# Kernel tuning notes

Measured on AMD Instinct MI355X. Metric: run time of the kernel, lower is better.

The kernel has to match this reference:

```python
import jax, jax.numpy as jnp
import numpy as np
from jax import lax

B, T, D_MODEL = 4, 2048, 2048
EXPAND, D_CONV = 2, 4
D_INNER = D_MODEL * EXPAND


def setup_inputs() -> dict:
    key = jax.random.key(0)
    ks = jax.random.split(key, 5)
    x = jax.random.normal(ks[0], (B, T, D_MODEL), dtype=jnp.float32)
    w_in = jax.random.normal(ks[1], (2 * D_INNER, D_MODEL), dtype=jnp.float32) * (D_MODEL ** -0.5)
    w_out = jax.random.normal(ks[2], (D_MODEL, D_INNER), dtype=jnp.float32) * (D_INNER ** -0.5)
    conv_w = jax.random.normal(ks[3], (D_INNER, 1, D_CONV), dtype=jnp.float32) * (D_CONV ** -0.5)
    conv_b = jax.random.normal(ks[4], (D_INNER,), dtype=jnp.float32) * 0.02
    D = jnp.ones((D_INNER,), dtype=jnp.float32)
    return {"x": x, "w_in": w_in, "w_out": w_out, "conv_w": conv_w, "conv_b": conv_b, "D": D}


def _forward(x, w_in, w_out, conv_w, conv_b, D):
    # in_proj: [B,T,C] @ [C, 2*d_inner]
    x_proj = jnp.einsum('btc,dc->btd', x, w_in)
    xi, gate = jnp.split(x_proj, 2, axis=-1)  # each [B,T,d_inner]
    # depthwise causal conv1d: torch pads both sides by d_conv-1 then truncates
    # output to first T positions -> equivalent to left-pad (d_conv-1), valid conv.
    xc = jnp.transpose(xi, (0, 2, 1))  # [B, d_inner, T]
    xc = lax.conv_general_dilated(
        xc, conv_w,
        window_strides=(1,),
        padding=[(D_CONV - 1, 0)],
        dimension_numbers=('NCH', 'OIH', 'NCH'),
        feature_group_count=D_INNER,
    ) + conv_b[None, :, None]
    xc = jnp.transpose(xc, (0, 2, 1))  # [B, T, d_inner]
    h = jax.nn.silu(xc) * D[None, None, :] * jax.nn.silu(gate)
    return jnp.einsum('btd,cd->btc', h, w_out)


def reference(x, w_in, w_out, conv_w, conv_b, D):
    return _forward(x, w_in, w_out, conv_w, conv_b, D)
```

## Files before the change

### kernel.cpp

```cpp
#include <hip/hip_runtime.h>
#include <hip/hip_bf16.h>
#include <stdint.h>


#define BT_TOTAL 8192
#define DM 2048
#define DI 4096

typedef __attribute__((ext_vector_type(8))) short short8;
typedef __attribute__((ext_vector_type(4))) float f32x4;

__device__ __forceinline__ void async_ld16(const void* g, void* l) {
    __builtin_amdgcn_global_load_lds(
        (__attribute__((address_space(1))) void*)g,
        (__attribute__((address_space(3))) void*)l,
        16, 0, 0);
}

template<bool OUT_BF16>
__global__ __launch_bounds__(256) void gemm_bt_kernel(
    const ushort* __restrict__ A, const ushort* __restrict__ B,
    void* __restrict__ Cp, int M, int N, int K)
{
    __shared__ ushort As[128 * 64];
    __shared__ ushort Bs[128 * 64];

    const int tid  = threadIdx.x;
    const int lane = tid & 63;
    const int wave = tid >> 6;
    const int wm   = (wave >> 1) * 64;
    const int wn   = (wave & 1) * 64;
    const int lr   = lane & 15;
    const int quad = lane >> 4;

    const int bm = blockIdx.y * 128;
    const int bn = blockIdx.x * 128;

    f32x4 acc[4][4];
#pragma unroll
    for (int i = 0; i < 4; ++i)
#pragma unroll
        for (int j = 0; j < 4; ++j)
            acc[i][j] = (f32x4){0.f, 0.f, 0.f, 0.f};

    const ushort* ag[4];
    const ushort* bg[4];
    ushort* al[4];
    ushort* bl[4];
#pragma unroll
    for (int t = 0; t < 4; ++t) {
        const int c  = tid + t * 256;
        const int r  = c >> 3;
        const int co = ((c & 7) ^ (r & 7)) * 8;
        ag[t] = A + (size_t)(bm + r) * (size_t)K + co;
        bg[t] = B + (size_t)(bn + r) * (size_t)K + co;
        al[t] = &As[c * 8];
        bl[t] = &Bs[c * 8];
    }

    for (int kk = 0; kk < K; kk += 64) {
        __syncthreads();
#pragma unroll
        for (int t = 0; t < 4; ++t) {
            async_ld16(ag[t] + kk, al[t]);
            async_ld16(bg[t] + kk, bl[t]);
        }
        __syncthreads();

#pragma unroll
        for (int ks = 0; ks < 64; ks += 32) {
            const int ca = ((quad + (ks >> 3)) ^ (lr & 7)) * 8;
            short8 af[4], bfr[4];
#pragma unroll
            for (int mt = 0; mt < 4; ++mt)
                af[mt] = *(const short8*)&As[(wm + mt * 16 + lr) * 64 + ca];
#pragma unroll
            for (int nt = 0; nt < 4; ++nt)
                bfr[nt] = *(const short8*)&Bs[(wn + nt * 16 + lr) * 64 + ca];
#pragma unroll
            for (int mt = 0; mt < 4; ++mt)
#pragma unroll
                for (int nt = 0; nt < 4; ++nt)
                    acc[mt][nt] = __builtin_amdgcn_mfma_f32_16x16x32_bf16(
                        af[mt], bfr[nt], acc[mt][nt], 0, 0, 0);
        }
    }

    const int row0 = bm + wm + quad * 4;
    const int col0 = bn + wn + lr;
    if (OUT_BF16) {
        __hip_bfloat16* C = (__hip_bfloat16*)Cp;
#pragma unroll
        for (int mt = 0; mt < 4; ++mt)
#pragma unroll
            for (int r = 0; r < 4; ++r) {
                const int gr = row0 + mt * 16 + r;
                __hip_bfloat16* Crow = C + (size_t)gr * (size_t)N + col0;
#pragma unroll
                for (int nt = 0; nt < 4; ++nt)
                    Crow[nt * 16] = __float2bfloat16(acc[mt][nt][r]);
            }
    } else {
        float* C = (float*)Cp;
#pragma unroll
        for (int mt = 0; mt < 4; ++mt)
#pragma unroll
            for (int r = 0; r < 4; ++r) {
                const int gr = row0 + mt * 16 + r;
                float* Crow = C + (size_t)gr * (size_t)N + col0;
#pragma unroll
                for (int nt = 0; nt < 4; ++nt)
                    Crow[nt * 16] = acc[mt][nt][r];
            }
    }
}

__global__ __launch_bounds__(256) void conv_silu_kernel(
    const __hip_bfloat16* __restrict__ xp,
    const float* __restrict__ cw,
    const float* __restrict__ cb,
    const float* __restrict__ Dv,
    __hip_bfloat16* __restrict__ h)
{
    const int idx = blockIdx.x * 256 + threadIdx.x;
    const int d  = idx & (DI - 1);
    const int bt = idx >> 12;
    const int t  = bt & 2047;

    const float gate = __bfloat162float(xp[(size_t)bt * (2 * DI) + DI + d]);

    float a = cb[d];
    const float4 w = *(const float4*)(cw + d * 4);
    const float wk[4] = {w.x, w.y, w.z, w.w};
#pragma unroll
    for (int k = 0; k < 4; ++k) {
        const int tt = t - 3 + k;
        if (tt >= 0)
            a += __bfloat162float(xp[(size_t)(bt - 3 + k) * (2 * DI) + d]) * wk[k];
    }
    const float sc = a / (1.f + __expf(-a));
    const float sg = gate / (1.f + __expf(-gate));
    h[(size_t)bt * DI + d] = __float2bfloat16(sc * Dv[d] * sg);
}

__global__ __launch_bounds__(256) void f32_to_bf16_x4(
    const float* __restrict__ in, __hip_bfloat16* __restrict__ out, int n4)
{
    const int i = blockIdx.x * 256 + threadIdx.x;
    if (i >= n4) return;
    const float4 v = *(const float4*)(in + (size_t)i * 4);
    union { __hip_bfloat16 hh[4]; ushort4 u; } cv;
    cv.hh[0] = __float2bfloat16(v.x);
    cv.hh[1] = __float2bfloat16(v.y);
    cv.hh[2] = __float2bfloat16(v.z);
    cv.hh[3] = __float2bfloat16(v.w);
    *(ushort4*)((ushort*)out + (size_t)i * 4) = cv.u;
}

extern "C" void kernel_launch(void* const* d_in, const int* in_sizes, int n_in,
                              void* d_out, int out_size, void* d_ws, size_t ws_size,
                              hipStream_t stream)
{
    const float* x     = (const float*)d_in[0];
    const float* w_in  = (const float*)d_in[1];
    const float* w_out = (const float*)d_in[2];
    const float* cw    = (const float*)d_in[3];
    const float* cb    = (const float*)d_in[4];
    const float* Dv    = (const float*)d_in[5];
    float* out = (float*)d_out;

    char* wsc = (char*)d_ws;
    __hip_bfloat16* xproj = (__hip_bfloat16*)wsc;
    __hip_bfloat16* xb    = (__hip_bfloat16*)(wsc + (size_t)134217728);
    __hip_bfloat16* winb  = (__hip_bfloat16*)(wsc + (size_t)134217728 + 33554432);
    __hip_bfloat16* hbuf  = (__hip_bfloat16*)(wsc + (size_t)134217728);
    __hip_bfloat16* woutb = (__hip_bfloat16*)(wsc + (size_t)201326592);

    f32_to_bf16_x4<<<(BT_TOTAL * DM / 4 + 255) / 256, 256, 0, stream>>>(x, xb, BT_TOTAL * DM / 4);
    f32_to_bf16_x4<<<(2 * DI * DM / 4 + 255) / 256, 256, 0, stream>>>(w_in, winb, 2 * DI * DM / 4);
    f32_to_bf16_x4<<<(DM * DI / 4 + 255) / 256, 256, 0, stream>>>(w_out, woutb, DM * DI / 4);

    gemm_bt_kernel<true><<<dim3(2 * DI / 128, BT_TOTAL / 128), 256, 0, stream>>>(
        (const ushort*)xb, (const ushort*)winb, xproj, BT_TOTAL, 2 * DI, DM);

    conv_silu_kernel<<<(BT_TOTAL * DI) / 256, 256, 0, stream>>>(xproj, cw, cb, Dv, hbuf);

    gemm_bt_kernel<false><<<dim3(DM / 128, BT_TOTAL / 128), 256, 0, stream>>>(
        (const ushort*)hbuf, (const ushort*)woutb, out, BT_TOTAL, DM, DI);
}
```

Baseline: 740.7 us.

## Use 32x32x16 MFMA in GEMMs and vectorize conv-SiLU kernel by eight

```diff
diff --git a/kernel.cpp b/kernel.cpp
--- a/kernel.cpp
+++ b/kernel.cpp
@@ -1,14 +1,15 @@
 #include <hip/hip_runtime.h>
 #include <hip/hip_bf16.h>
 #include <stdint.h>
+#include <string.h>
 
 
 #define BT_TOTAL 8192
 #define DM 2048
 #define DI 4096
 
-typedef __attribute__((ext_vector_type(8))) short short8;
-typedef __attribute__((ext_vector_type(4))) float f32x4;
+typedef __attribute__((ext_vector_type(8)))  short short8;
+typedef __attribute__((ext_vector_type(16))) float f32x16;
 
 __device__ __forceinline__ void async_ld16(const void* g, void* l) {
     __builtin_amdgcn_global_load_lds(
@@ -17,6 +18,16 @@
         16, 0, 0);
 }
 
+__device__ __forceinline__ float bf2f(ushort u) {
+    union { uint i; float f; } v; v.i = ((uint)u) << 16; return v.f;
+}
+
+__device__ __forceinline__ ushort f2bf_bits(float f) {
+    union { __hip_bfloat16 b; ushort u; } v;
+    v.b = __float2bfloat16(f);
+    return v.u;
+}
+
 template<bool OUT_BF16>
 __global__ __launch_bounds__(256) void gemm_bt_kernel(
     const ushort* __restrict__ A, const ushort* __restrict__ B,
@@ -30,21 +41,22 @@
     const int wave = tid >> 6;
     const int wm   = (wave >> 1) * 64;
     const int wn   = (wave & 1) * 64;
-    const int lr   = lane & 15;
-    const int quad = lane >> 4;
+    const int l31  = lane & 31;
+    const int half = lane >> 5;
 
     const int bm = blockIdx.y * 128;
     const int bn = blockIdx.x * 128;
 
-    f32x4 acc[4][4];
-#pragma unroll
-    for (int i = 0; i < 4; ++i)
-#pragma unroll
-        for (int j = 0; j < 4; ++j)
-            acc[i][j] = (f32x4){0.f, 0.f, 0.f, 0.f};
-
-    const ushort* ag[4];
-    const ushort* bg[4];
+    f32x16 acc[2][2];
+#pragma unroll
+    for (int i = 0; i < 2; ++i)
+#pragma unroll
+        for (int j = 0; j < 2; ++j)
+#pragma unroll
+            for (int r = 0; r < 16; ++r)
+                acc[i][j][r] = 0.f;
+
+    int aoff[4], boff[4];
     ushort* al[4];
     ushort* bl[4];
 #pragma unroll
@@ -52,95 +64,132 @@
         const int c  = tid + t * 256;
         const int r  = c >> 3;
         const int co = ((c & 7) ^ (r & 7)) * 8;
-        ag[t] = A + (size_t)(bm + r) * (size_t)K + co;
-        bg[t] = B + (size_t)(bn + r) * (size_t)K + co;
+        aoff[t] = (bm + r) * K + co;
+        boff[t] = (bn + r) * K + co;
         al[t] = &As[c * 8];
         bl[t] = &Bs[c * 8];
     }
 
+    const ushort* aP[8];
+    const ushort* bP[8];
+#pragma unroll
+    for (int s = 0; s < 4; ++s)
+#pragma unroll
+        for (int tt = 0; tt < 2; ++tt) {
+            const int rowA = wm + tt * 32 + l31;
+            const int rowB = wn + tt * 32 + l31;
+            const int q = s * 2 + half;
+            aP[s * 2 + tt] = &As[rowA * 64 + (q ^ (rowA & 7)) * 8];
+            bP[s * 2 + tt] = &Bs[rowB * 64 + (q ^ (rowB & 7)) * 8];
+        }
+
     for (int kk = 0; kk < K; kk += 64) {
+        const ushort* Ak = A + kk;
+        const ushort* Bk = B + kk;
         __syncthreads();
 #pragma unroll
         for (int t = 0; t < 4; ++t) {
-            async_ld16(ag[t] + kk, al[t]);
-            async_ld16(bg[t] + kk, bl[t]);
+            async_ld16(Ak + aoff[t], al[t]);
+            async_ld16(Bk + boff[t], bl[t]);
         }
         __syncthreads();
 
 #pragma unroll
-        for (int ks = 0; ks < 64; ks += 32) {
-            const int ca = ((quad + (ks >> 3)) ^ (lr & 7)) * 8;
-            short8 af[4], bfr[4];
-#pragma unroll
-            for (int mt = 0; mt < 4; ++mt)
-                af[mt] = *(const short8*)&As[(wm + mt * 16 + lr) * 64 + ca];
-#pragma unroll
-            for (int nt = 0; nt < 4; ++nt)
-                bfr[nt] = *(const short8*)&Bs[(wn + nt * 16 + lr) * 64 + ca];
-#pragma unroll
-            for (int mt = 0; mt < 4; ++mt)
-#pragma unroll
-                for (int nt = 0; nt < 4; ++nt)
-                    acc[mt][nt] = __builtin_amdgcn_mfma_f32_16x16x32_bf16(
-                        af[mt], bfr[nt], acc[mt][nt], 0, 0, 0);
-        }
-    }
-
-    const int row0 = bm + wm + quad * 4;
-    const int col0 = bn + wn + lr;
+        for (int s = 0; s < 4; ++s) {
+            short8 af[2], bf[2];
+#pragma unroll
+            for (int tt = 0; tt < 2; ++tt) {
+                af[tt] = *(const short8*)aP[s * 2 + tt];
+                bf[tt] = *(const short8*)bP[s * 2 + tt];
+            }
+#pragma unroll
+            for (int tm = 0; tm < 2; ++tm)
+#pragma unroll
+                for (int tn = 0; tn < 2; ++tn)
+                    acc[tm][tn] = __builtin_amdgcn_mfma_f32_32x32x16_bf16(
+                        af[tm], bf[tn], acc[tm][tn], 0, 0, 0);
+        }
+    }
+
+    const int col0  = bn + wn + l31;
+    const int rbase = bm + wm + 4 * half;
     if (OUT_BF16) {
         __hip_bfloat16* C = (__hip_bfloat16*)Cp;
 #pragma unroll
-        for (int mt = 0; mt < 4; ++mt)
-#pragma unroll
-            for (int r = 0; r < 4; ++r) {
-                const int gr = row0 + mt * 16 + r;
-                __hip_bfloat16* Crow = C + (size_t)gr * (size_t)N + col0;
-#pragma unroll
-                for (int nt = 0; nt < 4; ++nt)
-                    Crow[nt * 16] = __float2bfloat16(acc[mt][nt][r]);
-            }
+        for (int tm = 0; tm < 2; ++tm)
+#pragma unroll
+            for (int tn = 0; tn < 2; ++tn)
+#pragma unroll
+                for (int r = 0; r < 16; ++r) {
+                    const int row = rbase + tm * 32 + (r & 3) + 8 * (r >> 2);
+                    C[(size_t)row * (size_t)N + col0 + tn * 32] =
+                        __float2bfloat16(acc[tm][tn][r]);
+                }
     } else {
         float* C = (float*)Cp;
 #pragma unroll
-        for (int mt = 0; mt < 4; ++mt)
-#pragma unroll
-            for (int r = 0; r < 4; ++r) {
-                const int gr = row0 + mt * 16 + r;
-                float* Crow = C + (size_t)gr * (size_t)N + col0;
-#pragma unroll
-                for (int nt = 0; nt < 4; ++nt)
-                    Crow[nt * 16] = acc[mt][nt][r];
-            }
+        for (int tm = 0; tm < 2; ++tm)
+#pragma unroll
+            for (int tn = 0; tn < 2; ++tn)
+#pragma unroll
+                for (int r = 0; r < 16; ++r) {
+                    const int row = rbase + tm * 32 + (r & 3) + 8 * (r >> 2);
+                    C[(size_t)row * (size_t)N + col0 + tn * 32] = acc[tm][tn][r];
+                }
     }
 }
 
 __global__ __launch_bounds__(256) void conv_silu_kernel(
-    const __hip_bfloat16* __restrict__ xp,
+    const ushort* __restrict__ xp,
     const float* __restrict__ cw,
     const float* __restrict__ cb,
     const float* __restrict__ Dv,
-    __hip_bfloat16* __restrict__ h)
-{
-    const int idx = blockIdx.x * 256 + threadIdx.x;
-    const int d  = idx & (DI - 1);
-    const int bt = idx >> 12;
+    ushort* __restrict__ h)
+{
+    const int v  = blockIdx.x * 256 + threadIdx.x;
+    const int d8 = (v & 511) * 8;
+    const int bt = v >> 9;
     const int t  = bt & 2047;
 
-    const float gate = __bfloat162float(xp[(size_t)bt * (2 * DI) + DI + d]);
-
-    float a = cb[d];
-    const float4 w = *(const float4*)(cw + d * 4);
-    const float wk[4] = {w.x, w.y, w.z, w.w};
+    const uint4 gv = *(const uint4*)(xp + (size_t)bt * (2 * DI) + DI + d8);
+    uint4 tap[4];
 #pragma unroll
     for (int k = 0; k < 4; ++k) {
         const int tt = t - 3 + k;
         if (tt >= 0)
-            a += __bfloat162float(xp[(size_t)(bt - 3 + k) * (2 * DI) + d]) * wk[k];
-    }
-    const float sc = a / (1.f + __expf(-a));
-    const float sg = gate / (1.f + __expf(-gate));
-    h[(size_t)bt * DI + d] = __float2bfloat16(sc * Dv[d] * sg);
+            tap[k] = *(const uint4*)(xp + (size_t)(bt - 3 + k) * (2 * DI) + d8);
+        else
+            tap[k] = (uint4){0u, 0u, 0u, 0u};
+    }
+
+    const float4* cwv = (const float4*)(cw + (size_t)d8 * 4);
+    const float4  cb0 = *(const float4*)(cb + d8);
+    const float4  cb1 = *(const float4*)(cb + d8 + 4);
+    const float4  dv0 = *(const float4*)(Dv + d8);
+    const float4  dv1 = *(const float4*)(Dv + d8 + 4);
+    const float cbs[8] = {cb0.x, cb0.y, cb0.z, cb0.w, cb1.x, cb1.y, cb1.z, cb1.w};
+    const float dvs[8] = {dv0.x, dv0.y, dv0.z, dv0.w, dv1.x, dv1.y, dv1.z, dv1.w};
+
+    ushort res[8];
+#pragma unroll
+    for (int j = 0; j < 8; ++j) {
+        float a = cbs[j];
+        const float4 w = cwv[j];
+        const float wk[4] = {w.x, w.y, w.z, w.w};
+#pragma unroll
+        for (int k = 0; k < 4; ++k) {
+            const uint u = ((const uint*)&tap[k])[j >> 1];
+            const ushort us = (j & 1) ? (ushort)(u >> 16) : (ushort)(u & 0xffff);
+            a += bf2f(us) * wk[k];
+        }
+        const uint gu = ((const uint*)&gv)[j >> 1];
+        const ushort gs = (j & 1) ? (ushort)(gu >> 16) : (ushort)(gu & 0xffff);
+        const float g = bf2f(gs);
+        const float sc = a / (1.f + __expf(-a));
+        const float sg = g / (1.f + __expf(-g));
+        res[j] = f2bf_bits(sc * dvs[j] * sg);
+    }
+    *(uint4*)(h + (size_t)bt * DI + d8) = *(const uint4*)res;
 }
 
 __global__ __launch_bounds__(256) void f32_to_bf16_x4(
@@ -183,7 +232,8 @@
     gemm_bt_kernel<true><<<dim3(2 * DI / 128, BT_TOTAL / 128), 256, 0, stream>>>(
         (const ushort*)xb, (const ushort*)winb, xproj, BT_TOTAL, 2 * DI, DM);
 
-    conv_silu_kernel<<<(BT_TOTAL * DI) / 256, 256, 0, stream>>>(xproj, cw, cb, Dv, hbuf);
+    conv_silu_kernel<<<(BT_TOTAL * DI / 8) / 256, 256, 0, stream>>>(
+        (const ushort*)xproj, cw, cb, Dv, (ushort*)hbuf);
 
     gemm_bt_kernel<false><<<dim3(DM / 128, BT_TOTAL / 128), 256, 0, stream>>>(
         (const ushort*)hbuf, (const ushort*)woutb, out, BT_TOTAL, DM, DI);
```

New measurement: 719.3 us. -2.9%, faster.
